# Performance work log

Measured on AMD Instinct MI355X. Metric: run time of the kernel, lower is better.

## Reference

```python
import jax, jax.numpy as jnp
import numpy as np

T, H, I, E, TOP_K = 4096, 2048, 768, 16, 2


def _pack_i2s(tern):
    # tern: int8 in {-1,0,1}, shape [..., K] with K % 4 == 0
    m = (tern + 1).astype(jnp.uint8)  # map to {0,1,2}
    m = m.reshape(*tern.shape[:-1], -1, 4)
    return (m[..., 0] | (m[..., 1] << 2) | (m[..., 2] << 4) | (m[..., 3] << 6)).astype(jnp.uint8)


def _quantize_alpha(alpha):
    # per-column alpha -> int8 with global scale (quantize_alpha_int8)
    scale = jnp.maximum(jnp.abs(alpha).max(), 1e-8) / 127.0
    q = jnp.clip(jnp.round(alpha / scale), -128, 127).astype(jnp.int8)
    return q, scale.astype(jnp.float32)


def _unpack_i2s(packed, K, alpha):
    # packed: uint8 [..., N, K//4]; alpha: [..., K] per input column
    shifts = jnp.array([0, 2, 4, 6], dtype=jnp.uint8)
    ext = (packed[..., None] >> shifts) & jnp.uint8(3)  # [..., N, K//4, 4]
    vals = ext.reshape(*packed.shape[:-1], K).astype(jnp.float32) - 1.0  # {-1,0,1}
    return vals * alpha[..., None, :]


def setup_inputs() -> dict:
    key = jax.random.key(0)
    ks = jax.random.split(key, 6)
    x = jax.random.normal(ks[0], (T, H), dtype=jnp.float32)
    router_logits = jax.random.normal(ks[1], (T, E), dtype=jnp.float32)
    tern13 = jax.random.randint(ks[2], (E, 2 * I, H), -1, 2, dtype=jnp.int8)
    tern2 = jax.random.randint(ks[3], (E, H, I), -1, 2, dtype=jnp.int8)
    a13 = jax.random.uniform(ks[4], (E, H), minval=0.01, maxval=0.05, dtype=jnp.float32)
    a2 = jax.random.uniform(ks[5], (E, I), minval=0.01, maxval=0.05, dtype=jnp.float32)
    w13_alpha_q, w13_alpha_scale = _quantize_alpha(a13)
    w2_alpha_q, w2_alpha_scale = _quantize_alpha(a2)
    return {
        "x": x,
        "router_logits": router_logits,
        "w13_packed": _pack_i2s(tern13),
        "w13_alpha_q": w13_alpha_q,
        "w13_alpha_scale": w13_alpha_scale,
        "w2_packed": _pack_i2s(tern2),
        "w2_alpha_q": w2_alpha_q,
        "w2_alpha_scale": w2_alpha_scale,
    }


def reference(x, router_logits, w13_packed, w13_alpha_q, w13_alpha_scale,
              w2_packed, w2_alpha_q, w2_alpha_scale):
    # dequant int8 alphas, then dequant 2-bit ternary weights
    a13 = w13_alpha_q.astype(jnp.float32) * w13_alpha_scale  # [E, H]
    a2 = w2_alpha_q.astype(jnp.float32) * w2_alpha_scale     # [E, I]
    w13 = _unpack_i2s(w13_packed, H, a13)  # [E, 2I, H]
    w2 = _unpack_i2s(w2_packed, I, a2)     # [E, H, I]

    # top-k routing with renormalized softmax weights
    probs = jax.nn.softmax(router_logits, axis=-1)
    topw, topi = jax.lax.top_k(probs, TOP_K)           # [T, k]
    topw = topw / topw.sum(axis=-1, keepdims=True)
    combine = jnp.sum(jax.nn.one_hot(topi, E, dtype=x.dtype) * topw[..., None], axis=1)  # [T, E]

    # grouped expert matmuls (dense dispatch over experts)
    gu = jnp.einsum('th,enh->ten', x, w13)             # [T, E, 2I]
    gate, up = jnp.split(gu, 2, axis=-1)
    act = jax.nn.silu(gate) * up                       # [T, E, I]
    down = jnp.einsum('tei,ehi->teh', act, w2)         # [T, E, H]
    return jnp.einsum('te,teh->th', combine, down)     # [T, H]
```

## Files before the change

### kernel.cpp

```cpp
#include <hip/hip_runtime.h>
#include <stdint.h>

#define T_TOK 4096
#define HDIM  2048
#define IDIM  768
#define NEXP  16
#define NPAIR (T_TOK * 2)
#define PAIR_CAP (NPAIR + 256)

typedef float f32x4 __attribute__((ext_vector_type(4)));
typedef __bf16 bf16x8 __attribute__((ext_vector_type(8)));
typedef unsigned short u16x8 __attribute__((ext_vector_type(8)));
typedef unsigned int u32;
typedef const __attribute__((address_space(1))) u32* as1_u32p;
typedef __attribute__((address_space(3))) u32* as3_u32p;

__device__ __forceinline__ unsigned short f2bf(float f) {
  u32 u = __float_as_uint(f);
  u += 0x7FFFu + ((u >> 16) & 1u);
  return (unsigned short)(u >> 16);
}

__device__ __forceinline__ unsigned short tb(int m) {
  return m == 0 ? (unsigned short)0xBF80 : (m == 2 ? (unsigned short)0x3F80 : (unsigned short)0);
}

__device__ __forceinline__ f32x4 mfma16(bf16x8 a, bf16x8 b, f32x4 c) {
  return __builtin_amdgcn_mfma_f32_16x16x32_bf16(a, b, c, 0, 0, 0);
}

__global__ __launch_bounds__(256) void route_kernel(
    const float* __restrict__ logits, int* __restrict__ counts,
    int* __restrict__ t2i, float* __restrict__ t2w) {
  const int t = blockIdx.x * 256 + threadIdx.x;
  if (t >= T_TOK) return;
  const float* l = logits + t * NEXP;
  float m0 = -1e30f, m1 = -1e30f;
  int i0 = 0, i1 = 0;
#pragma unroll
  for (int j = 0; j < NEXP; ++j) {
    const float v = l[j];
    if (v > m0) { m1 = m0; i1 = i0; m0 = v; i0 = j; }
    else if (v > m1) { m1 = v; i1 = j; }
  }
  const float w0 = 1.0f / (1.0f + expf(m1 - m0));
  t2i[t] = i0 | (i1 << 8);
  t2w[t] = w0;
  atomicAdd(&counts[i0], 1);
  atomicAdd(&counts[i1], 1);
}

__global__ void scan_kernel(const int* __restrict__ counts,
                            int* __restrict__ offs, int* __restrict__ cursor) {
  if (threadIdx.x == 0) {
    int s = 0;
    for (int e = 0; e < NEXP; ++e) { offs[e] = s; cursor[e] = s; s += counts[e]; }
    offs[NEXP] = s;
  }
}

__global__ __launch_bounds__(256) void fill_kernel(
    const int* __restrict__ t2i, const float* __restrict__ t2w,
    int* __restrict__ cursor, int* __restrict__ pair_token,
    float* __restrict__ pair_wt, int* __restrict__ pair_eid,
    int* __restrict__ t2p0, int* __restrict__ t2p1) {
  const int t = blockIdx.x * 256 + threadIdx.x;
  if (t >= T_TOK) return;
  const int ii = t2i[t];
  const float w0 = t2w[t];
  const int i0 = ii & 255, i1 = (ii >> 8) & 255;
  const int p0 = atomicAdd(&cursor[i0], 1);
  pair_token[p0] = t; pair_wt[p0] = w0; pair_eid[p0] = i0;
  const int p1 = atomicAdd(&cursor[i1], 1);
  pair_token[p1] = t; pair_wt[p1] = 1.0f - w0; pair_eid[p1] = i1;
  t2p0[t] = p0; t2p1[t] = p1;
}

__global__ __launch_bounds__(256) void repack_kernel(
    const int* __restrict__ w, u32* __restrict__ o) {
  const int j0 = (blockIdx.x * 256 + threadIdx.x) * 4;
  const int4* w4 = (const int4*)w;
  uint4 r;
#pragma unroll
  for (int k = 0; k < 4; ++k) {
    const int4 a = w4[j0 + k];
    ((u32*)&r)[k] = (u32)(a.x & 255) | ((u32)(a.y & 255) << 8) |
                    ((u32)(a.z & 255) << 16) | ((u32)(a.w & 255) << 24);
  }
  ((uint4*)o)[blockIdx.x * 256 + threadIdx.x] = r;
}

__global__ __launch_bounds__(256) void xg_kernel(
    const float* __restrict__ x, const int* __restrict__ a13q,
    const float* __restrict__ s13p, const int* __restrict__ pair_token,
    const int* __restrict__ pair_eid, unsigned short* __restrict__ xg) {
  const int p = blockIdx.x;
  const int t = pair_token[p];
  const int e = pair_eid[p];
  const float s13 = *s13p;
  const int h0 = threadIdx.x * 8;
  const float* xp = x + (size_t)t * HDIM + h0;
  const int* ap = a13q + (size_t)e * HDIM + h0;
  const float4 x0 = ((const float4*)xp)[0];
  const float4 x1 = ((const float4*)xp)[1];
  const int4 a0 = ((const int4*)ap)[0];
  const int4 a1 = ((const int4*)ap)[1];
  u16x8 q;
  q[0] = f2bf(x0.x * (float)a0.x * s13);
  q[1] = f2bf(x0.y * (float)a0.y * s13);
  q[2] = f2bf(x0.z * (float)a0.z * s13);
  q[3] = f2bf(x0.w * (float)a0.w * s13);
  q[4] = f2bf(x1.x * (float)a1.x * s13);
  q[5] = f2bf(x1.y * (float)a1.y * s13);
  q[6] = f2bf(x1.z * (float)a1.z * s13);
  q[7] = f2bf(x1.w * (float)a1.w * s13);
  *(u16x8*)(xg + (size_t)p * HDIM + h0) = q;
}

__global__ __launch_bounds__(256, 4) void gemm1_kernel(
    const u32* __restrict__ wq13, const int* __restrict__ a2q,
    const float* __restrict__ s2p, const int* __restrict__ counts,
    const int* __restrict__ offs, const float* __restrict__ pair_wt,
    const unsigned short* __restrict__ xg, unsigned short* __restrict__ act) {
  const int id = blockIdx.x;
  const int xcd = id & 7, sblk = id >> 3;
  const int nT = sblk % 12;
  const int gg = (sblk / 12) * 8 + xcd;
  const int e = gg & 15, mT = gg >> 4;
  const int cnt = counts[e];
  if (mT * 128 >= cnt) return;
  const int base = offs[e];
  const int tid = threadIdx.x;

  __shared__ unsigned short sA[128 * 32];
  __shared__ unsigned short sB[128 * 36 + 8];
  __shared__ uint2 lut[256];

  {
    const int b = tid;
    const u32 lo = (u32)tb(b & 3) | ((u32)tb((b >> 2) & 3) << 16);
    const u32 hi = (u32)tb((b >> 4) & 3) | ((u32)tb((b >> 6) & 3) << 16);
    lut[b] = make_uint2(lo, hi);
  }
  __syncthreads();

  const int wave = tid >> 6, lane = tid & 63;
  const int wm = wave >> 1, wn = wave & 1;
  const int quad = lane >> 4, ln = lane & 15;

  const int bn = tid >> 1, bhalf = tid & 1;
  const int grow = (bn < 64) ? (nT * 64 + bn) : (IDIM + nT * 64 + (bn - 64));
  const u32* browp = wq13 + ((size_t)e * (2 * IDIM) + grow) * (HDIM / 16);
  unsigned short* sBw = sB + bn * 36 + (bhalf << 4);

  const int arow = lane >> 2;
  const int acol = (lane & 3) * 8;
  const size_t arow0 = (size_t)(base + mT * 128);

  f32x4 acc[4][4] = {};
  uint4 bq;

  for (int kt = 0; kt < HDIM / 32; ++kt) {
    if ((kt & 1) == 0) bq = *(const uint4*)(browp + kt * 2);
#pragma unroll
    for (int c = 0; c < 2; ++c) {
      const unsigned short* gp =
          xg + (arow0 + wave * 32 + c * 16 + arow) * HDIM + kt * 32 + acol;
      unsigned short* lp = sA + (wave * 32 + c * 16) * 32;
      __builtin_amdgcn_global_load_lds((as1_u32p)(const void*)gp, (as3_u32p)(void*)lp, 16, 0, 0);
    }
    {
      const u32 wb = (kt & 1) ? (bhalf ? bq.w : bq.z) : (bhalf ? bq.y : bq.x);
      const uint2 q0 = lut[wb & 255], q1 = lut[(wb >> 8) & 255];
      const uint2 q2 = lut[(wb >> 16) & 255], q3 = lut[wb >> 24];
      *(uint2*)(sBw + 0) = q0;
      *(uint2*)(sBw + 4) = q1;
      *(uint2*)(sBw + 8) = q2;
      *(uint2*)(sBw + 12) = q3;
    }
    __syncthreads();
    bf16x8 af[4], bf[4];
#pragma unroll
    for (int mi = 0; mi < 4; ++mi)
      af[mi] = *(const bf16x8*)(sA + (wm * 64 + mi * 16 + ln) * 32 + quad * 8);
#pragma unroll
    for (int ni = 0; ni < 4; ++ni) {
      const int brow = (ni < 2) ? (wn * 32 + ni * 16) : (64 + wn * 32 + (ni - 2) * 16);
      bf[ni] = *(const bf16x8*)(sB + (brow + ln) * 36 + quad * 8);
    }
#pragma unroll
    for (int ni = 0; ni < 4; ++ni)
#pragma unroll
      for (int mi = 0; mi < 4; ++mi) acc[mi][ni] = mfma16(af[mi], bf[ni], acc[mi][ni]);
    __syncthreads();
  }

  const float s2 = *s2p;
#pragma unroll
  for (int gi = 0; gi < 2; ++gi) {
    const int i = nT * 64 + wn * 32 + gi * 16 + ln;
    const float a2v = (float)a2q[e * IDIM + i] * s2;
#pragma unroll
    for (int mi = 0; mi < 4; ++mi) {
      const f32x4 g = acc[mi][gi];
      const f32x4 u = acc[mi][gi + 2];
#pragma unroll
      for (int r = 0; r < 4; ++r) {
        const int m = mT * 128 + wm * 64 + mi * 16 + quad * 4 + r;
        if (m < cnt) {
          const float wt = pair_wt[base + m];
          const float gv = g[r];
          const float av = gv / (1.0f + __expf(-gv)) * u[r] * a2v * wt;
          act[(size_t)(base + m) * IDIM + i] = f2bf(av);
        }
      }
    }
  }
}

template <bool ATOMIC>
__global__ __launch_bounds__(256, 4) void gemm2_kernel(
    const u32* __restrict__ wq2, const int* __restrict__ counts,
    const int* __restrict__ offs, const int* __restrict__ pair_token,
    const unsigned short* __restrict__ act, float* __restrict__ outp,
    unsigned short* __restrict__ down) {
  const int id = blockIdx.x;
  const int xcd = id & 7, sblk = id >> 3;
  const int nT = sblk & 15;
  const int gg = (sblk >> 4) * 8 + xcd;
  const int e = gg & 15, mT = gg >> 4;
  const int cnt = counts[e];
  if (mT * 128 >= cnt) return;
  const int base = offs[e];
  const int tid = threadIdx.x;

  __shared__ unsigned short sA[128 * 32];
  __shared__ unsigned short sB[128 * 36 + 8];
  __shared__ uint2 lut[256];
  __shared__ int stok[128];

  {
    const int b = tid;
    const u32 lo = (u32)tb(b & 3) | ((u32)tb((b >> 2) & 3) << 16);
    const u32 hi = (u32)tb((b >> 4) & 3) | ((u32)tb((b >> 6) & 3) << 16);
    lut[b] = make_uint2(lo, hi);
    if (ATOMIC && tid < 128) {
      const int m = mT * 128 + tid;
      stok[tid] = (m < cnt) ? pair_token[base + m] : 0;
    }
  }
  __syncthreads();

  const int wave = tid >> 6, lane = tid & 63;
  const int wm = wave >> 1, wn = wave & 1;
  const int quad = lane >> 4, ln = lane & 15;

  const int bn = tid >> 1, bhalf = tid & 1;
  const u32* browp = wq2 + ((size_t)e * HDIM + nT * 128 + bn) * (IDIM / 16);
  unsigned short* sBw = sB + bn * 36 + (bhalf << 4);

  const int arow = lane >> 2;
  const int acol = (lane & 3) * 8;
  const size_t arow0 = (size_t)(base + mT * 128);

  f32x4 acc[4][4] = {};
  uint4 bq;

  for (int kt = 0; kt < IDIM / 32; ++kt) {
    if ((kt & 1) == 0) bq = *(const uint4*)(browp + kt * 2);
#pragma unroll
    for (int c = 0; c < 2; ++c) {
      const unsigned short* gp =
          act + (arow0 + wave * 32 + c * 16 + arow) * IDIM + kt * 32 + acol;
      unsigned short* lp = sA + (wave * 32 + c * 16) * 32;
      __builtin_amdgcn_global_load_lds((as1_u32p)(const void*)gp, (as3_u32p)(void*)lp, 16, 0, 0);
    }
    {
      const u32 wb = (kt & 1) ? (bhalf ? bq.w : bq.z) : (bhalf ? bq.y : bq.x);
      const uint2 q0 = lut[wb & 255], q1 = lut[(wb >> 8) & 255];
      const uint2 q2 = lut[(wb >> 16) & 255], q3 = lut[wb >> 24];
      *(uint2*)(sBw + 0) = q0;
      *(uint2*)(sBw + 4) = q1;
      *(uint2*)(sBw + 8) = q2;
      *(uint2*)(sBw + 12) = q3;
    }
    __syncthreads();
    bf16x8 af[4], bf[4];
#pragma unroll
    for (int mi = 0; mi < 4; ++mi)
      af[mi] = *(const bf16x8*)(sA + (wm * 64 + mi * 16 + ln) * 32 + quad * 8);
#pragma unroll
    for (int ni = 0; ni < 4; ++ni)
      bf[ni] = *(const bf16x8*)(sB + (wn * 64 + ni * 16 + ln) * 36 + quad * 8);
#pragma unroll
    for (int ni = 0; ni < 4; ++ni)
#pragma unroll
      for (int mi = 0; mi < 4; ++mi) acc[mi][ni] = mfma16(af[mi], bf[ni], acc[mi][ni]);
    __syncthreads();
  }

#pragma unroll
  for (int mi = 0; mi < 4; ++mi) {
#pragma unroll
    for (int r = 0; r < 4; ++r) {
      const int ml = wm * 64 + mi * 16 + quad * 4 + r;
      const int m = mT * 128 + ml;
      if (m < cnt) {
        const int col0 = nT * 128 + wn * 64;
        if (ATOMIC) {
          float* orow = outp + (size_t)stok[ml] * HDIM + col0;
#pragma unroll
          for (int ni = 0; ni < 4; ++ni)
            atomicAdd(orow + ni * 16 + ln, acc[mi][ni][r]);
        } else {
          unsigned short* drow = down + (size_t)(base + m) * HDIM + col0;
#pragma unroll
          for (int ni = 0; ni < 4; ++ni)
            drow[ni * 16 + ln] = f2bf(acc[mi][ni][r]);
        }
      }
    }
  }
}

__global__ __launch_bounds__(256) void combine_kernel(
    const int* __restrict__ t2p0, const int* __restrict__ t2p1,
    const unsigned short* __restrict__ down, float* __restrict__ out) {
  const int t = blockIdx.x;
  const int h = threadIdx.x * 8;
  const u16x8 a = *(const u16x8*)(down + (size_t)t2p0[t] * HDIM + h);
  const u16x8 b = *(const u16x8*)(down + (size_t)t2p1[t] * HDIM + h);
  f32x4 o0, o1;
#pragma unroll
  for (int j = 0; j < 4; ++j) {
    o0[j] = __uint_as_float((u32)a[j] << 16) + __uint_as_float((u32)b[j] << 16);
    o1[j] = __uint_as_float((u32)a[j + 4] << 16) + __uint_as_float((u32)b[j + 4] << 16);
  }
  float* o = out + (size_t)t * HDIM + h;
  *(f32x4*)(o) = o0;
  *(f32x4*)(o + 4) = o1;
}

extern "C" void kernel_launch(void* const* d_in, const int* in_sizes, int n_in,
                              void* d_out, int out_size, void* d_ws, size_t ws_size,
                              hipStream_t stream) {
  const float* x      = (const float*)d_in[0];
  const float* logits = (const float*)d_in[1];
  const int*   w13p   = (const int*)d_in[2];
  const int*   a13q   = (const int*)d_in[3];
  const float* s13    = (const float*)d_in[4];
  const int*   w2p    = (const int*)d_in[5];
  const int*   a2q    = (const int*)d_in[6];
  const float* s2     = (const float*)d_in[7];
  float* out = (float*)d_out;

  char* ws = (char*)d_ws;
  int*   counts     = (int*)(ws + 0);
  int*   cursor     = (int*)(ws + 64);
  int*   offs       = (int*)(ws + 128);
  int*   t2i        = (int*)(ws + 256);
  float* t2w        = (float*)(ws + 256 + 4 * T_TOK);
  int*   t2p0       = (int*)(ws + 256 + 8 * T_TOK);
  int*   t2p1       = (int*)(ws + 256 + 12 * T_TOK);
  int*   pair_token = (int*)(ws + 256 + 16 * T_TOK);
  float* pair_wt    = (float*)(ws + 256 + 16 * T_TOK + 4 * PAIR_CAP);
  int*   pair_eid   = (int*)(ws + 256 + 16 * T_TOK + 8 * PAIR_CAP);
  const size_t hdr_end = ((size_t)(256 + 16 * T_TOK + 12 * PAIR_CAP) + 255) & ~(size_t)255;

  const size_t n32_13 = (size_t)NEXP * 2 * IDIM * (HDIM / 16);
  const size_t n32_2  = (size_t)NEXP * HDIM * (IDIM / 16);
  const size_t rp13_b = n32_13 * 4, rp2_b = n32_2 * 4;
  const size_t xg_b   = (size_t)PAIR_CAP * HDIM * 2;
  const size_t act_b  = (size_t)PAIR_CAP * IDIM * 2;
  const size_t dwn_b  = (size_t)PAIR_CAP * HDIM * 2;

  const size_t need_B = hdr_end + rp13_b + rp2_b + xg_b + act_b;
  const size_t need_A = need_B + dwn_b;

  u32* rp13 = (u32*)(ws + hdr_end);
  u32* rp2  = (u32*)(ws + hdr_end + rp13_b);
  unsigned short* xg  = (unsigned short*)(ws + hdr_end + rp13_b + rp2_b);
  unsigned short* act = (unsigned short*)(ws + hdr_end + rp13_b + rp2_b + xg_b);

  hipMemsetAsync(counts, 0, 256, stream);
  route_kernel<<<T_TOK / 256, 256, 0, stream>>>(logits, counts, t2i, t2w);
  scan_kernel<<<1, 64, 0, stream>>>(counts, offs, cursor);
  fill_kernel<<<T_TOK / 256, 256, 0, stream>>>(t2i, t2w, cursor, pair_token, pair_wt,
                                               pair_eid, t2p0, t2p1);
  repack_kernel<<<(int)(n32_13 / 1024), 256, 0, stream>>>(w13p, rp13);
  repack_kernel<<<(int)(n32_2 / 1024), 256, 0, stream>>>(w2p, rp2);
  xg_kernel<<<NPAIR, 256, 0, stream>>>(x, a13q, s13, pair_token, pair_eid, xg);

  gemm1_kernel<<<6144, 256, 0, stream>>>(rp13, a2q, s2, counts, offs, pair_wt, xg, act);

  if (ws_size >= need_A) {
    unsigned short* down = (unsigned short*)(ws + need_B);
    gemm2_kernel<false><<<8192, 256, 0, stream>>>(rp2, counts, offs, pair_token,
                                                  act, nullptr, down);
    combine_kernel<<<T_TOK, 256, 0, stream>>>(t2p0, t2p1, down, out);
  } else {
    hipMemsetAsync(out, 0, (size_t)out_size * sizeof(float), stream);
    gemm2_kernel<true><<<8192, 256, 0, stream>>>(rp2, counts, offs, pair_token,
                                                 act, out, nullptr);
  }
}
```

Baseline: 351.1 us.

## Load A fragments directly to registers and double-buffer dequantized B in LDS

```diff
diff --git a/kernel.cpp b/kernel.cpp
--- a/kernel.cpp
+++ b/kernel.cpp
@@ -12,8 +12,6 @@
 typedef __bf16 bf16x8 __attribute__((ext_vector_type(8)));
 typedef unsigned short u16x8 __attribute__((ext_vector_type(8)));
 typedef unsigned int u32;
-typedef const __attribute__((address_space(1))) u32* as1_u32p;
-typedef __attribute__((address_space(3))) u32* as3_u32p;
 
 __device__ __forceinline__ unsigned short f2bf(float f) {
   u32 u = __float_as_uint(f);
@@ -117,7 +115,26 @@
   *(u16x8*)(xg + (size_t)p * HDIM + h0) = q;
 }
 
-__global__ __launch_bounds__(256, 4) void gemm1_kernel(
+#define STAGE_B(buf, wb)                                                   \
+  {                                                                        \
+    unsigned short* dst = &sB[buf][sBoff];                                 \
+    const uint2 q0 = lut[(wb) & 255], q1 = lut[((wb) >> 8) & 255];         \
+    const uint2 q2 = lut[((wb) >> 16) & 255], q3 = lut[(wb) >> 24];        \
+    *(uint2*)(dst + 0) = q0;                                               \
+    *(uint2*)(dst + 4) = q1;                                               \
+    *(uint2*)(dst + 8) = q2;                                               \
+    *(uint2*)(dst + 12) = q3;                                              \
+  }
+
+#define LOAD_A(dst, kt)                                                    \
+  {                                                                        \
+    dst[0] = *(const bf16x8*)(ap0 + (kt) * 32);                            \
+    dst[1] = *(const bf16x8*)(ap1 + (kt) * 32);                            \
+    dst[2] = *(const bf16x8*)(ap2 + (kt) * 32);                            \
+    dst[3] = *(const bf16x8*)(ap3 + (kt) * 32);                            \
+  }
+
+__global__ __launch_bounds__(256, 3) void gemm1_kernel(
     const u32* __restrict__ wq13, const int* __restrict__ a2q,
     const float* __restrict__ s2p, const int* __restrict__ counts,
     const int* __restrict__ offs, const float* __restrict__ pair_wt,
@@ -132,8 +149,7 @@
   const int base = offs[e];
   const int tid = threadIdx.x;
 
-  __shared__ unsigned short sA[128 * 32];
-  __shared__ unsigned short sB[128 * 36 + 8];
+  __shared__ unsigned short sB[2][128 * 36 + 8];
   __shared__ uint2 lut[256];
 
   {
@@ -150,49 +166,55 @@
 
   const int bn = tid >> 1, bhalf = tid & 1;
   const int grow = (bn < 64) ? (nT * 64 + bn) : (IDIM + nT * 64 + (bn - 64));
-  const u32* browp = wq13 + ((size_t)e * (2 * IDIM) + grow) * (HDIM / 16);
-  unsigned short* sBw = sB + bn * 36 + (bhalf << 4);
-
-  const int arow = lane >> 2;
-  const int acol = (lane & 3) * 8;
+  const u32* browp = wq13 + ((size_t)e * (2 * IDIM) + grow) * (HDIM / 16) + bhalf;
+  const int sBoff = bn * 36 + (bhalf << 4);
+
   const size_t arow0 = (size_t)(base + mT * 128);
+  const unsigned short* ap0 = xg + (arow0 + wm * 64 + ln) * HDIM + quad * 8;
+  const unsigned short* ap1 = ap0 + 16 * (size_t)HDIM;
+  const unsigned short* ap2 = ap0 + 32 * (size_t)HDIM;
+  const unsigned short* ap3 = ap0 + 48 * (size_t)HDIM;
 
   f32x4 acc[4][4] = {};
-  uint4 bq;
-
-  for (int kt = 0; kt < HDIM / 32; ++kt) {
-    if ((kt & 1) == 0) bq = *(const uint4*)(browp + kt * 2);
-#pragma unroll
-    for (int c = 0; c < 2; ++c) {
-      const unsigned short* gp =
-          xg + (arow0 + wave * 32 + c * 16 + arow) * HDIM + kt * 32 + acol;
-      unsigned short* lp = sA + (wave * 32 + c * 16) * 32;
-      __builtin_amdgcn_global_load_lds((as1_u32p)(const void*)gp, (as3_u32p)(void*)lp, 16, 0, 0);
-    }
+  bf16x8 afA[4], afB[4];
+
+  u32 wb = browp[0];
+  STAGE_B(0, wb);
+  u32 wbn = browp[2];
+  LOAD_A(afA, 0);
+  __syncthreads();
+
+#define G1_MFMA(buf, af)                                                          \
+  {                                                                               \
+    bf16x8 b0 = *(const bf16x8*)(&sB[buf][(wn * 32 + ln) * 36 + quad * 8]);       \
+    bf16x8 b1 = *(const bf16x8*)(&sB[buf][(wn * 32 + 16 + ln) * 36 + quad * 8]);  \
+    bf16x8 b2 = *(const bf16x8*)(&sB[buf][(64 + wn * 32 + ln) * 36 + quad * 8]);  \
+    bf16x8 b3 = *(const bf16x8*)(&sB[buf][(64 + wn * 32 + 16 + ln) * 36 + quad * 8]); \
+    _Pragma("unroll") for (int mi = 0; mi < 4; ++mi) {                            \
+      acc[mi][0] = mfma16(af[mi], b0, acc[mi][0]);                                \
+      acc[mi][1] = mfma16(af[mi], b1, acc[mi][1]);                                \
+      acc[mi][2] = mfma16(af[mi], b2, acc[mi][2]);                                \
+      acc[mi][3] = mfma16(af[mi], b3, acc[mi][3]);                                \
+    }                                                                             \
+  }
+
+  for (int kt = 0; kt < HDIM / 32; kt += 2) {
     {
-      const u32 wb = (kt & 1) ? (bhalf ? bq.w : bq.z) : (bhalf ? bq.y : bq.x);
-      const uint2 q0 = lut[wb & 255], q1 = lut[(wb >> 8) & 255];
-      const uint2 q2 = lut[(wb >> 16) & 255], q3 = lut[wb >> 24];
-      *(uint2*)(sBw + 0) = q0;
-      *(uint2*)(sBw + 4) = q1;
-      *(uint2*)(sBw + 8) = q2;
-      *(uint2*)(sBw + 12) = q3;
-    }
-    __syncthreads();
-    bf16x8 af[4], bf[4];
-#pragma unroll
-    for (int mi = 0; mi < 4; ++mi)
-      af[mi] = *(const bf16x8*)(sA + (wm * 64 + mi * 16 + ln) * 32 + quad * 8);
-#pragma unroll
-    for (int ni = 0; ni < 4; ++ni) {
-      const int brow = (ni < 2) ? (wn * 32 + ni * 16) : (64 + wn * 32 + (ni - 2) * 16);
-      bf[ni] = *(const bf16x8*)(sB + (brow + ln) * 36 + quad * 8);
-    }
-#pragma unroll
-    for (int ni = 0; ni < 4; ++ni)
-#pragma unroll
-      for (int mi = 0; mi < 4; ++mi) acc[mi][ni] = mfma16(af[mi], bf[ni], acc[mi][ni]);
-    __syncthreads();
+      STAGE_B(1, wbn);
+      wbn = browp[(kt + 2) * 2];
+      LOAD_A(afB, kt + 1);
+      G1_MFMA(0, afA);
+      __syncthreads();
+    }
+    {
+      if (kt + 2 < HDIM / 32) {
+        STAGE_B(0, wbn);
+        wbn = browp[(kt + 3) * 2];
+        LOAD_A(afA, kt + 2);
+      }
+      G1_MFMA(1, afB);
+      __syncthreads();
+    }
   }
 
   const float s2 = *s2p;
@@ -218,11 +240,9 @@
   }
 }
 
-template <bool ATOMIC>
-__global__ __launch_bounds__(256, 4) void gemm2_kernel(
+__global__ __launch_bounds__(256, 3) void gemm2_kernel(
     const u32* __restrict__ wq2, const int* __restrict__ counts,
-    const int* __restrict__ offs, const int* __restrict__ pair_token,
-    const unsigned short* __restrict__ act, float* __restrict__ outp,
+    const int* __restrict__ offs, const unsigned short* __restrict__ act,
     unsigned short* __restrict__ down) {
   const int id = blockIdx.x;
   const int xcd = id & 7, sblk = id >> 3;
@@ -234,20 +254,14 @@
   const int base = offs[e];
   const int tid = threadIdx.x;
 
-  __shared__ unsigned short sA[128 * 32];
-  __shared__ unsigned short sB[128 * 36 + 8];
+  __shared__ unsigned short sB[2][128 * 36 + 8];
   __shared__ uint2 lut[256];
-  __shared__ int stok[128];
 
   {
     const int b = tid;
     const u32 lo = (u32)tb(b & 3) | ((u32)tb((b >> 2) & 3) << 16);
     const u32 hi = (u32)tb((b >> 4) & 3) | ((u32)tb((b >> 6) & 3) << 16);
     lut[b] = make_uint2(lo, hi);
-    if (ATOMIC && tid < 128) {
-      const int m = mT * 128 + tid;
-      stok[tid] = (m < cnt) ? pair_token[base + m] : 0;
-    }
   }
   __syncthreads();
 
@@ -256,47 +270,55 @@
   const int quad = lane >> 4, ln = lane & 15;
 
   const int bn = tid >> 1, bhalf = tid & 1;
-  const u32* browp = wq2 + ((size_t)e * HDIM + nT * 128 + bn) * (IDIM / 16);
-  unsigned short* sBw = sB + bn * 36 + (bhalf << 4);
-
-  const int arow = lane >> 2;
-  const int acol = (lane & 3) * 8;
+  const u32* browp = wq2 + ((size_t)e * HDIM + nT * 128 + bn) * (IDIM / 16) + bhalf;
+  const int sBoff = bn * 36 + (bhalf << 4);
+
   const size_t arow0 = (size_t)(base + mT * 128);
+  const unsigned short* ap0 = act + (arow0 + wm * 64 + ln) * IDIM + quad * 8;
+  const unsigned short* ap1 = ap0 + 16 * (size_t)IDIM;
+  const unsigned short* ap2 = ap0 + 32 * (size_t)IDIM;
+  const unsigned short* ap3 = ap0 + 48 * (size_t)IDIM;
 
   f32x4 acc[4][4] = {};
-  uint4 bq;
-
-  for (int kt = 0; kt < IDIM / 32; ++kt) {
-    if ((kt & 1) == 0) bq = *(const uint4*)(browp + kt * 2);
-#pragma unroll
-    for (int c = 0; c < 2; ++c) {
-      const unsigned short* gp =
-          act + (arow0 + wave * 32 + c * 16 + arow) * IDIM + kt * 32 + acol;
-      unsigned short* lp = sA + (wave * 32 + c * 16) * 32;
-      __builtin_amdgcn_global_load_lds((as1_u32p)(const void*)gp, (as3_u32p)(void*)lp, 16, 0, 0);
-    }
+  bf16x8 afA[4], afB[4];
+
+  u32 wb = browp[0];
+  STAGE_B(0, wb);
+  u32 wbn = browp[2];
+  LOAD_A(afA, 0);
+  __syncthreads();
+
+#define G2_MFMA(buf, af)                                                          \
+  {                                                                               \
+    bf16x8 b0 = *(const bf16x8*)(&sB[buf][(wn * 64 + ln) * 36 + quad * 8]);       \
+    bf16x8 b1 = *(const bf16x8*)(&sB[buf][(wn * 64 + 16 + ln) * 36 + quad * 8]);  \
+    bf16x8 b2 = *(const bf16x8*)(&sB[buf][(wn * 64 + 32 + ln) * 36 + quad * 8]);  \
+    bf16x8 b3 = *(const bf16x8*)(&sB[buf][(wn * 64 + 48 + ln) * 36 + quad * 8]);  \
+    _Pragma("unroll") for (int mi = 0; mi < 4; ++mi) {                            \
+      acc[mi][0] = mfma16(af[mi], b0, acc[mi][0]);                                \
+      acc[mi][1] = mfma16(af[mi], b1, acc[mi][1]);                                \
+      acc[mi][2] = mfma16(af[mi], b2, acc[mi][2]);                                \
+      acc[mi][3] = mfma16(af[mi], b3, acc[mi][3]);                                \
+    }                                                                             \
+  }
+
+  for (int kt = 0; kt < IDIM / 32; kt += 2) {
     {
-      const u32 wb = (kt & 1) ? (bhalf ? bq.w : bq.z) : (bhalf ? bq.y : bq.x);
-      const uint2 q0 = lut[wb & 255], q1 = lut[(wb >> 8) & 255];
-      const uint2 q2 = lut[(wb >> 16) & 255], q3 = lut[wb >> 24];
-      *(uint2*)(sBw + 0) = q0;
-      *(uint2*)(sBw + 4) = q1;
-      *(uint2*)(sBw + 8) = q2;
-      *(uint2*)(sBw + 12) = q3;
-    }
-    __syncthreads();
-    bf16x8 af[4], bf[4];
-#pragma unroll
-    for (int mi = 0; mi < 4; ++mi)
-      af[mi] = *(const bf16x8*)(sA + (wm * 64 + mi * 16 + ln) * 32 + quad * 8);
-#pragma unroll
-    for (int ni = 0; ni < 4; ++ni)
-      bf[ni] = *(const bf16x8*)(sB + (wn * 64 + ni * 16 + ln) * 36 + quad * 8);
-#pragma unroll
-    for (int ni = 0; ni < 4; ++ni)
-#pragma unroll
-      for (int mi = 0; mi < 4; ++mi) acc[mi][ni] = mfma16(af[mi], bf[ni], acc[mi][ni]);
-    __syncthreads();
+      STAGE_B(1, wbn);
+      wbn = browp[(kt + 2) * 2];
+      LOAD_A(afB, kt + 1);
+      G2_MFMA(0, afA);
+      __syncthreads();
+    }
+    {
+      if (kt + 2 < IDIM / 32) {
+        STAGE_B(0, wbn);
+        wbn = browp[(kt + 3) * 2];
+        LOAD_A(afA, kt + 2);
+      }
+      G2_MFMA(1, afB);
+      __syncthreads();
+    }
   }
 
 #pragma unroll
@@ -306,18 +328,10 @@
       const int ml = wm * 64 + mi * 16 + quad * 4 + r;
       const int m = mT * 128 + ml;
       if (m < cnt) {
-        const int col0 = nT * 128 + wn * 64;
-        if (ATOMIC) {
-          float* orow = outp + (size_t)stok[ml] * HDIM + col0;
-#pragma unroll
-          for (int ni = 0; ni < 4; ++ni)
-            atomicAdd(orow + ni * 16 + ln, acc[mi][ni][r]);
-        } else {
-          unsigned short* drow = down + (size_t)(base + m) * HDIM + col0;
-#pragma unroll
-          for (int ni = 0; ni < 4; ++ni)
-            drow[ni * 16 + ln] = f2bf(acc[mi][ni][r]);
-        }
+        unsigned short* drow = down + (size_t)(base + m) * HDIM + nT * 128 + wn * 64;
+#pragma unroll
+        for (int ni = 0; ni < 4; ++ni)
+          drow[ni * 16 + ln] = f2bf(acc[mi][ni][r]);
       }
     }
   }
@@ -371,16 +385,12 @@
   const size_t n32_2  = (size_t)NEXP * HDIM * (IDIM / 16);
   const size_t rp13_b = n32_13 * 4, rp2_b = n32_2 * 4;
   const size_t xg_b   = (size_t)PAIR_CAP * HDIM * 2;
-  const size_t act_b  = (size_t)PAIR_CAP * IDIM * 2;
-  const size_t dwn_b  = (size_t)PAIR_CAP * HDIM * 2;
-
-  const size_t need_B = hdr_end + rp13_b + rp2_b + xg_b + act_b;
-  const size_t need_A = need_B + dwn_b;
 
   u32* rp13 = (u32*)(ws + hdr_end);
   u32* rp2  = (u32*)(ws + hdr_end + rp13_b);
   unsigned short* xg  = (unsigned short*)(ws + hdr_end + rp13_b + rp2_b);
   unsigned short* act = (unsigned short*)(ws + hdr_end + rp13_b + rp2_b + xg_b);
+  unsigned short* down = xg;
 
   hipMemsetAsync(counts, 0, 256, stream);
   route_kernel<<<T_TOK / 256, 256, 0, stream>>>(logits, counts, t2i, t2w);
@@ -392,15 +402,6 @@
   xg_kernel<<<NPAIR, 256, 0, stream>>>(x, a13q, s13, pair_token, pair_eid, xg);
 
   gemm1_kernel<<<6144, 256, 0, stream>>>(rp13, a2q, s2, counts, offs, pair_wt, xg, act);
-
-  if (ws_size >= need_A) {
-    unsigned short* down = (unsigned short*)(ws + need_B);
-    gemm2_kernel<false><<<8192, 256, 0, stream>>>(rp2, counts, offs, pair_token,
-                                                  act, nullptr, down);
-    combine_kernel<<<T_TOK, 256, 0, stream>>>(t2p0, t2p1, down, out);
-  } else {
-    hipMemsetAsync(out, 0, (size_t)out_size * sizeof(float), stream);
-    gemm2_kernel<true><<<8192, 256, 0, stream>>>(rp2, counts, offs, pair_token,
-                                                 act, out, nullptr);
-  }
-}
+  gemm2_kernel<<<8192, 256, 0, stream>>>(rp2, counts, offs, act, down);
+  combine_kernel<<<T_TOK, 256, 0, stream>>>(t2p0, t2p1, down, out);
+}
```

After: 447.8 us. 27.5% more time.
